# Kernel tuning notes

Measured on AMD Instinct MI355X. Metric: run time of the kernel, lower is better.

## Reference

```python
import jax, jax.numpy as jnp
import numpy as np
import math

H = 16
D_MODEL = 1024
D_K = 64
BS = 8
SEQ = 1024


def setup_inputs() -> dict:
    key = jax.random.key(0)
    ks = jax.random.split(key, 13)
    s = 1.0 / math.sqrt(D_MODEL)
    inp = {
        "q": jax.random.normal(ks[0], (BS, SEQ, D_MODEL), dtype=jnp.float32),
        "k": jax.random.normal(ks[1], (BS, SEQ, D_MODEL), dtype=jnp.float32),
        "v": jax.random.normal(ks[2], (BS, SEQ, D_MODEL), dtype=jnp.float32),
        "mask": jax.random.randint(ks[3], (BS, SEQ, SEQ), 0, 2, dtype=jnp.int32),
        "Wq": jax.random.normal(ks[4], (D_MODEL, D_MODEL), dtype=jnp.float32) * s,
        "bq": jax.random.normal(ks[5], (D_MODEL,), dtype=jnp.float32) * s,
        "Wk": jax.random.normal(ks[6], (D_MODEL, D_MODEL), dtype=jnp.float32) * s,
        "bk": jax.random.normal(ks[7], (D_MODEL,), dtype=jnp.float32) * s,
        "Wv": jax.random.normal(ks[8], (D_MODEL, D_MODEL), dtype=jnp.float32) * s,
        "bv": jax.random.normal(ks[9], (D_MODEL,), dtype=jnp.float32) * s,
        "Wo": jax.random.normal(ks[10], (D_MODEL, D_MODEL), dtype=jnp.float32) * s,
        "bo": jax.random.normal(ks[11], (D_MODEL,), dtype=jnp.float32) * s,
    }
    return inp


def reference(q, k, v, mask, Wq, bq, Wk, bk, Wv, bv, Wo, bo):
    bs, seq, _ = q.shape
    # projections, split heads: [b, h, s, dk]
    def proj(x, W, b):
        y = x @ W + b
        return y.reshape(bs, seq, H, D_K).transpose(0, 2, 1, 3)
    qh = proj(q, Wq, bq)
    kh = proj(k, Wk, bk)
    vh = proj(v, Wv, bv)
    # scaled dot-product attention (dropout is identity in eval mode)
    scores = jnp.einsum("bhqd,bhkd->bhqk", qh, kh) / math.sqrt(D_K)
    scores = jnp.where(mask[:, None, :, :] == 0, jnp.float32(-1e9), scores)
    attn = jax.nn.softmax(scores, axis=-1)
    ctx = jnp.einsum("bhqk,bhkd->bhqd", attn, vh)
    concat = ctx.transpose(0, 2, 1, 3).reshape(bs, seq, D_MODEL)
    return concat @ Wo + bo
```

## Files before the change

### kernel.cpp

```cpp
#include <hip/hip_runtime.h>
#include <hip/hip_bf16.h>
#include <math.h>

#define HN 16
#define DM 1024
#define DK 64
#define BSZ 8
#define SEQL 1024

typedef __attribute__((ext_vector_type(8))) short bf16x8;
typedef __attribute__((ext_vector_type(4))) short short4v;
typedef __attribute__((ext_vector_type(4))) float f32x4;

__device__ __forceinline__ short f2bf(float f) {
    union { float f; unsigned u; } x; x.f = f;
    unsigned u = x.u + 0x7FFFu + ((x.u >> 16) & 1u);
    return (short)(u >> 16);
}

__global__ __launch_bounds__(256) void transpose_cast(const float* __restrict__ W,
                                                      short* __restrict__ Wt) {
    __shared__ float tile[32][33];
    const int t = threadIdx.x;
    const int k0 = blockIdx.x * 32, n0 = blockIdx.y * 32;
    const int c = t & 31, r = t >> 5;
    #pragma unroll
    for (int p = 0; p < 4; ++p)
        tile[r + 8 * p][c] = W[(size_t)(k0 + r + 8 * p) * DM + n0 + c];
    __syncthreads();
    #pragma unroll
    for (int p = 0; p < 4; ++p)
        Wt[(size_t)(n0 + r + 8 * p) * DM + k0 + c] = f2bf(tile[c][r + 8 * p]);
}

template <int MODE>
__global__ __launch_bounds__(256) void gemm_mfma(const void* __restrict__ Ap,
                                                 const short* __restrict__ Wt,
                                                 const float* __restrict__ bias,
                                                 void* __restrict__ Cp) {
    __shared__ __attribute__((aligned(16))) short As[128][40];
    __shared__ __attribute__((aligned(16))) short Bs[128][40];
    const int t = threadIdx.x;
    const int lane = t & 63, wv = t >> 6;
    const int wm = (wv >> 1) * 64, wn = (wv & 1) * 64;
    const int quad = lane >> 4, l15 = lane & 15;
    const int tileM = blockIdx.x * 128, tileN = blockIdx.y * 128;
    const size_t zoff = (size_t)blockIdx.z * DM * SEQL;

    f32x4 acc[4][4];
    #pragma unroll
    for (int i = 0; i < 4; ++i)
        #pragma unroll
        for (int j = 0; j < 4; ++j) acc[i][j] = {0.f, 0.f, 0.f, 0.f};

    for (int k0 = 0; k0 < DM; k0 += 32) {
        if (MODE == 0) {
            const float* A = (const float*)Ap + zoff;
            const int r0 = t >> 3, c4 = (t & 7) * 4;
            #pragma unroll
            for (int p = 0; p < 4; ++p) {
                int row = r0 + 32 * p;
                float4 v = *(const float4*)(A + (size_t)(tileM + row) * DM + k0 + c4);
                short4v s4 = {f2bf(v.x), f2bf(v.y), f2bf(v.z), f2bf(v.w)};
                *(short4v*)&As[row][c4] = s4;
            }
        } else {
            const short* A = (const short*)Ap + zoff;
            const int r0 = t >> 2, c8 = (t & 3) * 8;
            #pragma unroll
            for (int p = 0; p < 2; ++p) {
                int row = r0 + 64 * p;
                *(bf16x8*)&As[row][c8] =
                    *(const bf16x8*)(A + (size_t)(tileM + row) * DM + k0 + c8);
            }
        }
        {
            const int r0 = t >> 2, c8 = (t & 3) * 8;
            #pragma unroll
            for (int p = 0; p < 2; ++p) {
                int row = r0 + 64 * p;
                *(bf16x8*)&Bs[row][c8] =
                    *(const bf16x8*)(Wt + (size_t)(tileN + row) * DM + k0 + c8);
            }
        }
        __syncthreads();
        bf16x8 a[4], b[4];
        #pragma unroll
        for (int i = 0; i < 4; ++i) a[i] = *(const bf16x8*)&As[wm + i * 16 + l15][quad * 8];
        #pragma unroll
        for (int j = 0; j < 4; ++j) b[j] = *(const bf16x8*)&Bs[wn + j * 16 + l15][quad * 8];
        #pragma unroll
        for (int i = 0; i < 4; ++i)
            #pragma unroll
            for (int j = 0; j < 4; ++j)
                acc[i][j] = __builtin_amdgcn_mfma_f32_16x16x32_bf16(a[i], b[j], acc[i][j], 0, 0, 0);
        __syncthreads();
    }

    #pragma unroll
    for (int i = 0; i < 4; ++i)
        #pragma unroll
        for (int j = 0; j < 4; ++j)
            #pragma unroll
            for (int rr = 0; rr < 4; ++rr) {
                int row = tileM + wm + i * 16 + quad * 4 + rr;
                int col = tileN + wn + j * 16 + l15;
                float v = acc[i][j][rr] + bias[col];
                if (MODE == 0) {
                    short* C = (short*)Cp + zoff;
                    C[((size_t)(col >> 6) * SEQL + row) * DK + (col & 63)] = f2bf(v);
                } else {
                    float* C = (float*)Cp + zoff;
                    C[(size_t)row * DM + col] = v;
                }
            }
}

__global__ __launch_bounds__(256) void attn_mfma(const short* __restrict__ Qw,
                                                 const short* __restrict__ Kw,
                                                 const short* __restrict__ Vw,
                                                 const int* __restrict__ mask,
                                                 short* __restrict__ ctx) {
    __shared__ __attribute__((aligned(16))) short Qs[64][72];
    __shared__ __attribute__((aligned(16))) short Ks[64][72];
    __shared__ __attribute__((aligned(16))) short Vs[64][72];
    __shared__ __attribute__((aligned(16))) short Ps[4][16][72];
    const int t = threadIdx.x;
    const int lane = t & 63, w = t >> 6;
    const int quad = lane >> 4, l15 = lane & 15;
    const int q0 = blockIdx.x * 64;
    const int h = blockIdx.y;
    const size_t zoff = (size_t)blockIdx.z * DM * SEQL;
    const short* Qb = Qw + zoff + (size_t)h * SEQL * DK;
    const short* Kb = Kw + zoff + (size_t)h * SEQL * DK;
    const short* Vb = Vw + zoff + (size_t)h * SEQL * DK;
    const int* mb = mask + (size_t)blockIdx.z * SEQL * SEQL;

    #pragma unroll
    for (int p = 0; p < 2; ++p) {
        int cc = t + 256 * p;
        int row = cc >> 3, off = (cc & 7) * 8;
        *(bf16x8*)&Qs[row][off] = *(const bf16x8*)(Qb + (size_t)(q0 + row) * DK + off);
    }

    f32x4 o[4];
    #pragma unroll
    for (int td = 0; td < 4; ++td) o[td] = {0.f, 0.f, 0.f, 0.f};
    float Lacc[4] = {0.f, 0.f, 0.f, 0.f};

    for (int j0 = 0; j0 < SEQL; j0 += 64) {
        #pragma unroll
        for (int p = 0; p < 2; ++p) {
            int cc = t + 256 * p;
            int row = cc >> 3, off = (cc & 7) * 8;
            *(bf16x8*)&Ks[row][off] = *(const bf16x8*)(Kb + (size_t)(j0 + row) * DK + off);
        }
        {
            int r = t >> 2, c16 = (t & 3) * 16;
            bf16x8 v0 = *(const bf16x8*)(Vb + (size_t)(j0 + r) * DK + c16);
            bf16x8 v1 = *(const bf16x8*)(Vb + (size_t)(j0 + r) * DK + c16 + 8);
            #pragma unroll
            for (int u = 0; u < 8; ++u) Vs[c16 + u][r] = v0[u];
            #pragma unroll
            for (int u = 0; u < 8; ++u) Vs[c16 + 8 + u][r] = v1[u];
        }
        __syncthreads();

        #pragma unroll
        for (int tn = 0; tn < 4; ++tn) {
            f32x4 s = {0.f, 0.f, 0.f, 0.f};
            #pragma unroll
            for (int ks = 0; ks < 2; ++ks) {
                bf16x8 aq = *(const bf16x8*)&Qs[w * 16 + l15][ks * 32 + quad * 8];
                bf16x8 bk = *(const bf16x8*)&Ks[tn * 16 + l15][ks * 32 + quad * 8];
                s = __builtin_amdgcn_mfma_f32_16x16x32_bf16(aq, bk, s, 0, 0, 0);
            }
            #pragma unroll
            for (int rr = 0; rr < 4; ++rr) {
                int rq = q0 + w * 16 + quad * 4 + rr;
                int cj = j0 + tn * 16 + l15;
                float p = mb[(size_t)rq * SEQL + cj] ? __expf(s[rr] * 0.125f) : 0.0f;
                Lacc[rr] += p;
                Ps[w][quad * 4 + rr][tn * 16 + l15] = f2bf(p);
            }
        }
        __syncthreads();

        #pragma unroll
        for (int td = 0; td < 4; ++td)
            #pragma unroll
            for (int ks = 0; ks < 2; ++ks) {
                bf16x8 ap = *(const bf16x8*)&Ps[w][l15][ks * 32 + quad * 8];
                bf16x8 bv = *(const bf16x8*)&Vs[td * 16 + l15][ks * 32 + quad * 8];
                o[td] = __builtin_amdgcn_mfma_f32_16x16x32_bf16(ap, bv, o[td], 0, 0, 0);
            }
        __syncthreads();
    }

    #pragma unroll
    for (int rr = 0; rr < 4; ++rr) {
        float l = Lacc[rr];
        l += __shfl_xor(l, 1);
        l += __shfl_xor(l, 2);
        l += __shfl_xor(l, 4);
        l += __shfl_xor(l, 8);
        Lacc[rr] = 1.0f / l;
    }
    short* cb = ctx + zoff;
    #pragma unroll
    for (int td = 0; td < 4; ++td)
        #pragma unroll
        for (int rr = 0; rr < 4; ++rr) {
            int rq = q0 + w * 16 + quad * 4 + rr;
            int cd = h * 64 + td * 16 + l15;
            cb[(size_t)rq * DM + cd] = f2bf(o[td][rr] * Lacc[rr]);
        }
}

extern "C" void kernel_launch(void* const* d_in, const int* in_sizes, int n_in,
                              void* d_out, int out_size, void* d_ws, size_t ws_size,
                              hipStream_t stream) {
    const float* q  = (const float*)d_in[0];
    const float* k  = (const float*)d_in[1];
    const float* v  = (const float*)d_in[2];
    const int* mask = (const int*)d_in[3];
    const float* Wq = (const float*)d_in[4];
    const float* bq = (const float*)d_in[5];
    const float* Wk = (const float*)d_in[6];
    const float* bk = (const float*)d_in[7];
    const float* Wv = (const float*)d_in[8];
    const float* bv = (const float*)d_in[9];
    const float* Wo = (const float*)d_in[10];
    const float* bo = (const float*)d_in[11];
    float* out = (float*)d_out;

    const size_t MEL = (size_t)1024 * 1024;
    short* wsb = (short*)d_ws;
    short* Wqt = wsb;
    short* Wkt = wsb + MEL;
    short* Wvt = wsb + 2 * MEL;
    short* Wot = wsb + 3 * MEL;

    transpose_cast<<<dim3(32, 32), 256, 0, stream>>>(Wq, Wqt);
    transpose_cast<<<dim3(32, 32), 256, 0, stream>>>(Wk, Wkt);
    transpose_cast<<<dim3(32, 32), 256, 0, stream>>>(Wv, Wvt);
    transpose_cast<<<dim3(32, 32), 256, 0, stream>>>(Wo, Wot);

    const bool full = ws_size >= ((size_t)80 << 20);
    const int zdim = full ? BSZ : 1;
    const int iters = full ? 1 : BSZ;

    const size_t bufEl = full ? 8 * MEL : MEL;
    short* Qw  = wsb + 4 * MEL;
    short* Kw  = Qw + bufEl;
    short* Vw  = Kw + bufEl;
    short* ctx = Vw + bufEl;

    for (int it = 0; it < iters; ++it) {
        const float* qb = q + (size_t)it * MEL;
        const float* kb = k + (size_t)it * MEL;
        const float* vb = v + (size_t)it * MEL;
        const int* mbp  = mask + (size_t)it * MEL;
        float* ob       = out + (size_t)it * MEL;

        gemm_mfma<0><<<dim3(8, 8, zdim), 256, 0, stream>>>(qb, Wqt, bq, Qw);
        gemm_mfma<0><<<dim3(8, 8, zdim), 256, 0, stream>>>(kb, Wkt, bk, Kw);
        gemm_mfma<0><<<dim3(8, 8, zdim), 256, 0, stream>>>(vb, Wvt, bv, Vw);

        attn_mfma<<<dim3(16, 16, zdim), 256, 0, stream>>>(Qw, Kw, Vw, mbp, ctx);

        gemm_mfma<1><<<dim3(8, 8, zdim), 256, 0, stream>>>(ctx, Wot, bo, ob);
    }
}
```

Measured before the change: 440.8 us.

## Pack mask to bits, write V pre-transposed, drop a barrier in attention

Adds a pre-pass that packs the int32 mask into 64-bit ballot words, so the attention kernel reads one word per row per key tile instead of 16 int32 values per thread per tile. This is meant to cut the 32 MB of mask traffic that every head re-reads. The V projection now writes V in transposed [head][dk][seq] layout, so attention loads it with vector stores instead of scattered shared-memory transposes. One __syncthreads between the P write and the PV MFMA is removed because each wave uses only its own Ps slice. The workspace tiering is also reworked to allow partial batch chunking.

```diff
diff --git a/kernel.cpp b/kernel.cpp
--- a/kernel.cpp
+++ b/kernel.cpp
@@ -1,6 +1,5 @@
 #include <hip/hip_runtime.h>
 #include <hip/hip_bf16.h>
-#include <math.h>
 
 #define HN 16
 #define DM 1024
@@ -31,6 +30,13 @@
     #pragma unroll
     for (int p = 0; p < 4; ++p)
         Wt[(size_t)(n0 + r + 8 * p) * DM + k0 + c] = f2bf(tile[c][r + 8 * p]);
+}
+
+__global__ __launch_bounds__(256) void pack_mask(const int* __restrict__ mask,
+                                                 unsigned long long* __restrict__ bits) {
+    size_t i = (size_t)blockIdx.x * 256 + threadIdx.x;
+    unsigned long long b = __ballot(mask[i] != 0);
+    if ((threadIdx.x & 63) == 0) bits[i >> 6] = b;
 }
 
 template <int MODE>
@@ -54,7 +60,7 @@
         for (int j = 0; j < 4; ++j) acc[i][j] = {0.f, 0.f, 0.f, 0.f};
 
     for (int k0 = 0; k0 < DM; k0 += 32) {
-        if (MODE == 0) {
+        if (MODE != 1) {
             const float* A = (const float*)Ap + zoff;
             const int r0 = t >> 3, c4 = (t & 7) * 4;
             #pragma unroll
@@ -109,17 +115,21 @@
                 if (MODE == 0) {
                     short* C = (short*)Cp + zoff;
                     C[((size_t)(col >> 6) * SEQL + row) * DK + (col & 63)] = f2bf(v);
-                } else {
+                } else if (MODE == 1) {
                     float* C = (float*)Cp + zoff;
                     C[(size_t)row * DM + col] = v;
+                } else {
+                    short* C = (short*)Cp + zoff;
+                    C[(size_t)col * SEQL + row] = f2bf(v);
                 }
             }
 }
 
+template <bool USE_BITS>
 __global__ __launch_bounds__(256) void attn_mfma(const short* __restrict__ Qw,
                                                  const short* __restrict__ Kw,
-                                                 const short* __restrict__ Vw,
-                                                 const int* __restrict__ mask,
+                                                 const short* __restrict__ Vt,
+                                                 const void* __restrict__ maskp,
                                                  short* __restrict__ ctx) {
     __shared__ __attribute__((aligned(16))) short Qs[64][72];
     __shared__ __attribute__((aligned(16))) short Ks[64][72];
@@ -133,8 +143,7 @@
     const size_t zoff = (size_t)blockIdx.z * DM * SEQL;
     const short* Qb = Qw + zoff + (size_t)h * SEQL * DK;
     const short* Kb = Kw + zoff + (size_t)h * SEQL * DK;
-    const short* Vb = Vw + zoff + (size_t)h * SEQL * DK;
-    const int* mb = mask + (size_t)blockIdx.z * SEQL * SEQL;
+    const short* Vb = Vt + zoff + (size_t)h * DK * SEQL;
 
     #pragma unroll
     for (int p = 0; p < 2; ++p) {
@@ -154,17 +163,18 @@
             int cc = t + 256 * p;
             int row = cc >> 3, off = (cc & 7) * 8;
             *(bf16x8*)&Ks[row][off] = *(const bf16x8*)(Kb + (size_t)(j0 + row) * DK + off);
-        }
-        {
-            int r = t >> 2, c16 = (t & 3) * 16;
-            bf16x8 v0 = *(const bf16x8*)(Vb + (size_t)(j0 + r) * DK + c16);
-            bf16x8 v1 = *(const bf16x8*)(Vb + (size_t)(j0 + r) * DK + c16 + 8);
-            #pragma unroll
-            for (int u = 0; u < 8; ++u) Vs[c16 + u][r] = v0[u];
-            #pragma unroll
-            for (int u = 0; u < 8; ++u) Vs[c16 + 8 + u][r] = v1[u];
+            *(bf16x8*)&Vs[row][off] = *(const bf16x8*)(Vb + (size_t)row * SEQL + j0 + off);
         }
         __syncthreads();
+
+        unsigned long long mw[4];
+        if (USE_BITS) {
+            const unsigned long long* mb =
+                (const unsigned long long*)maskp + (size_t)blockIdx.z * SEQL * 16;
+            #pragma unroll
+            for (int rr = 0; rr < 4; ++rr)
+                mw[rr] = mb[(size_t)(q0 + w * 16 + quad * 4 + rr) * 16 + (j0 >> 6)];
+        }
 
         #pragma unroll
         for (int tn = 0; tn < 4; ++tn) {
@@ -177,15 +187,18 @@
             }
             #pragma unroll
             for (int rr = 0; rr < 4; ++rr) {
-                int rq = q0 + w * 16 + quad * 4 + rr;
-                int cj = j0 + tn * 16 + l15;
-                float p = mb[(size_t)rq * SEQL + cj] ? __expf(s[rr] * 0.125f) : 0.0f;
+                bool keep;
+                if (USE_BITS) {
+                    keep = (mw[rr] >> (tn * 16 + l15)) & 1ull;
+                } else {
+                    const int* mb = (const int*)maskp + (size_t)blockIdx.z * SEQL * SEQL;
+                    keep = mb[(size_t)(q0 + w * 16 + quad * 4 + rr) * SEQL + j0 + tn * 16 + l15] != 0;
+                }
+                float p = keep ? __expf(s[rr] * 0.125f) : 0.0f;
                 Lacc[rr] += p;
                 Ps[w][quad * 4 + rr][tn * 16 + l15] = f2bf(p);
             }
         }
-        __syncthreads();
-
         #pragma unroll
         for (int td = 0; td < 4; ++td)
             #pragma unroll
@@ -234,40 +247,57 @@
     const float* bo = (const float*)d_in[11];
     float* out = (float*)d_out;
 
+    const size_t MB = (size_t)1 << 20;
     const size_t MEL = (size_t)1024 * 1024;
-    short* wsb = (short*)d_ws;
-    short* Wqt = wsb;
-    short* Wkt = wsb + MEL;
-    short* Wvt = wsb + 2 * MEL;
-    short* Wot = wsb + 3 * MEL;
+    char* base = (char*)d_ws;
+
+    short* Wqt = (short*)(base + 0 * 2 * MB);
+    short* Wkt = (short*)(base + 1 * 2 * MB);
+    short* Wvt = (short*)(base + 2 * 2 * MB);
+    short* Wot = (short*)(base + 3 * 2 * MB);
+
+    int zdim;
+    bool use_bits;
+    if      (ws_size >= 74 * MB) { zdim = 8; use_bits = true; }
+    else if (ws_size >= 42 * MB) { zdim = 4; use_bits = true; }
+    else if (ws_size >= 26 * MB) { zdim = 2; use_bits = true; }
+    else if (ws_size >= 18 * MB) { zdim = 1; use_bits = true; }
+    else                         { zdim = 1; use_bits = false; }
+
+    unsigned long long* bits = (unsigned long long*)(base + 8 * MB);
+    char* bufs = base + (use_bits ? 9 : 8) * MB;
+    const size_t bufB = (size_t)zdim * 2 * MB;
+    short* Qw  = (short*)(bufs);
+    short* Kw  = (short*)(bufs + bufB);
+    short* Vw  = (short*)(bufs + 2 * bufB);
+    short* ctx = (short*)(bufs + 3 * bufB);
 
     transpose_cast<<<dim3(32, 32), 256, 0, stream>>>(Wq, Wqt);
     transpose_cast<<<dim3(32, 32), 256, 0, stream>>>(Wk, Wkt);
     transpose_cast<<<dim3(32, 32), 256, 0, stream>>>(Wv, Wvt);
     transpose_cast<<<dim3(32, 32), 256, 0, stream>>>(Wo, Wot);
-
-    const bool full = ws_size >= ((size_t)80 << 20);
-    const int zdim = full ? BSZ : 1;
-    const int iters = full ? 1 : BSZ;
-
-    const size_t bufEl = full ? 8 * MEL : MEL;
-    short* Qw  = wsb + 4 * MEL;
-    short* Kw  = Qw + bufEl;
-    short* Vw  = Kw + bufEl;
-    short* ctx = Vw + bufEl;
-
+    if (use_bits)
+        pack_mask<<<(BSZ * SEQL * SEQL) / 256, 256, 0, stream>>>(mask, bits);
+
+    const int iters = BSZ / zdim;
     for (int it = 0; it < iters; ++it) {
-        const float* qb = q + (size_t)it * MEL;
-        const float* kb = k + (size_t)it * MEL;
-        const float* vb = v + (size_t)it * MEL;
-        const int* mbp  = mask + (size_t)it * MEL;
-        float* ob       = out + (size_t)it * MEL;
+        const size_t boff = (size_t)it * zdim * MEL;
+        const float* qb = q + boff;
+        const float* kb = k + boff;
+        const float* vb = v + boff;
+        float* ob = out + boff;
+        const void* mb = use_bits
+            ? (const void*)(bits + (size_t)it * zdim * SEQL * 16)
+            : (const void*)(mask + (size_t)it * zdim * SEQL * SEQL);
 
         gemm_mfma<0><<<dim3(8, 8, zdim), 256, 0, stream>>>(qb, Wqt, bq, Qw);
         gemm_mfma<0><<<dim3(8, 8, zdim), 256, 0, stream>>>(kb, Wkt, bk, Kw);
-        gemm_mfma<0><<<dim3(8, 8, zdim), 256, 0, stream>>>(vb, Wvt, bv, Vw);
-
-        attn_mfma<<<dim3(16, 16, zdim), 256, 0, stream>>>(Qw, Kw, Vw, mbp, ctx);
+        gemm_mfma<2><<<dim3(8, 8, zdim), 256, 0, stream>>>(vb, Wvt, bv, Vw);
+
+        if (use_bits)
+            attn_mfma<true><<<dim3(16, 16, zdim), 256, 0, stream>>>(Qw, Kw, Vw, mb, ctx);
+        else
+            attn_mfma<false><<<dim3(16, 16, zdim), 256, 0, stream>>>(Qw, Kw, Vw, mb, ctx);
 
         gemm_mfma<1><<<dim3(8, 8, zdim), 256, 0, stream>>>(ctx, Wot, bo, ob);
     }
```

Result: no change. 437.4 us (-0.8%).
